# Optimization experiments

Hardware: AMD Instinct MI355X
Metric: run time of the kernel (lower is better)

Reference implementation:

```python
import jax, jax.numpy as jnp
import numpy as np
from jax import lax

T, C_IN, H, W = 15, 6, 160, 160
F1, K1, THR1 = 30, 5, 15.0
F2, K2, THR2 = 250, 3, 10.0
KWTA2, RADIUS2 = 8, 1


def conv2d(x, w):
    # x: [T, Cin, H, W] (time occupies the batch slot, SpykeTorch style); w: [Cout, Cin, k, k]
    return lax.conv_general_dilated(x, w, (1, 1), 'VALID',
                                    dimension_numbers=('NCHW', 'OIHW', 'NCHW'))


def fire(pot, thr):
    # torch.nn.functional.threshold_(pot, thr, 0): keep strictly-greater values
    p = jnp.where(pot > thr, pot, 0.0)
    return jnp.sign(p), p


def max_pool(x, k, s):
    return lax.reduce_window(x, -jnp.inf, lax.max, (1, 1, k, k), (1, 1, s, s), 'VALID')


def pad_hw(x, p):
    return jnp.pad(x, ((0, 0), (0, 0), (p, p), (p, p)))


def pointwise_inhibition(pot):
    # pot: [T, F, H, W] thresholded potentials (cumulative spike encoding over T).
    # At each spatial position keep only the feature that spiked earliest (via the
    # per-timestep max feature at the first spiking timestep); zero all others.
    t = pot.shape[0]
    max_val = pot.max(axis=1, keepdims=True)      # [T,1,H,W]
    max_idx = pot.argmax(axis=1, keepdims=True)   # [T,1,H,W]
    clamp = jnp.sign(max_val)                     # spike indicator of per-position max
    first_t = jnp.clip((t - clamp.sum(axis=0, keepdims=True)).astype(jnp.int32), 0, t - 1)
    last = clamp[-1:]                             # [1,1,H,W]: 1 if position ever spiked
    winner_f = jnp.take_along_axis(max_idx, first_t, axis=0)  # [1,1,H,W]
    f_range = jnp.arange(pot.shape[1]).reshape(1, -1, 1, 1)
    coef = jnp.where(f_range == winner_f, last, 0.0)          # scatter_(1, winners, last)
    return pot * coef


def get_k_winners(pot, spikes, kwta, radius):
    # Faithful jit-friendly version of sf.get_k_winners: rank by (spiked-early, potential),
    # iteratively pick the max, suppress its whole feature map and a (2r+1)^2 spatial
    # window across all features (NMS-like).
    t, f, h, w = pot.shape
    first_t = jnp.clip((t - spikes.sum(axis=0)).astype(jnp.int32), 0, t - 1)  # [F,H,W]
    values = jnp.take_along_axis(pot, first_t[None], axis=0)[0]  # earliest potential per neuron
    truncated = spikes * values[None]
    v = truncated.max() * t
    total = (truncated + spikes * v).sum(axis=0)  # [F,H,W]
    hs, ws = jnp.arange(h), jnp.arange(w)

    def step(tot, _):
        idx = jnp.argmax(tot)
        val = tot.reshape(-1)[idx]
        valid = val != 0.0
        fi = idx // (h * w)
        hi = (idx % (h * w)) // w
        wi = idx % w
        tot = jnp.where(valid, tot.at[fi].set(0.0), tot)  # block the winning feature
        sp = (jnp.abs(hs - hi)[:, None] <= radius) & (jnp.abs(ws - wi)[None, :] <= radius)
        tot = jnp.where(valid & sp[None], 0.0, tot)       # columnar spatial inhibition
        win = jnp.where(valid, jnp.stack([fi, hi, wi]), -1)
        return tot, win

    _, winners = lax.scan(step, total, None, length=kwta)
    return winners  # [kwta, 3] (feature, row, col), -1 rows = no winner


def setup_inputs():
    key = jax.random.key(0)
    k1, k2, k3 = jax.random.split(key, 3)
    # Cumulative spike-wave input: each (c,h,w) neuron fires at most once; spikes accumulate over T.
    u = jax.random.uniform(k1, (T, C_IN, H, W), dtype=jnp.float32)
    data = jnp.clip(jnp.cumsum((u < 0.05).astype(jnp.float32), axis=0), 0.0, 1.0)
    W1 = 0.8 + 0.05 * jax.random.normal(k2, (F1, C_IN, K1, K1), dtype=jnp.float32)
    W2 = 0.8 + 0.05 * jax.random.normal(k3, (F2, F1, K2, K2), dtype=jnp.float32)
    return {"data": data, "W1": W1, "W2": W2}


def reference(data, W1, W2):
    x = pad_hw(data, 2)                                  # sf.pad(data, (2,2,2,2))
    spike1, _ = fire(conv2d(x, W1), THR1)                # conv1 + fire(thr=15)
    inp2 = pad_hw(max_pool(spike1, 2, 2), 1)             # pool(2,2) + pad(1,1,1,1)
    _, pot2 = fire(conv2d(inp2, W2), THR2)               # conv2 + fire(thr=10)
    pot2 = pointwise_inhibition(pot2)                    # lateral inhibition
    spike2 = jnp.sign(pot2)
    winners = get_k_winners(pot2, spike2, KWTA2, RADIUS2)  # k=8, r=1 spatial k-WTA
    return spike2, pot2, winners
```

## Files before the change

kernel.cpp:

```cpp
#include <hip/hip_runtime.h>
#include <cstdint>

#define T_    15
#define C1    6
#define F1    30
#define THR1  15.0f
#define F2    250
#define THR2  10.0f
#define WP    80
#define NLOC  6400
#define KWTA  8
#define P1R   164
#define P1S   (164*164)
#define P2R   84
#define P2S   (84*84)
#define POT_OFF 24000000
#define WIN_OFF 48000000

typedef unsigned long long u64;
typedef unsigned short u16;
typedef short s16x8 __attribute__((ext_vector_type(8)));
typedef float f32x4 __attribute__((ext_vector_type(4)));

static __device__ __forceinline__ u16 f2bf(float x) {
    unsigned u = __float_as_uint(x);
    return (u16)((u + 0x7FFF + ((u >> 16) & 1)) >> 16);
}
static __device__ __forceinline__ float bf2f(u16 h) {
    return __uint_as_float(((unsigned)h) << 16);
}

__global__ void k_pad(const float* __restrict__ data, float* __restrict__ P1) {
    int idx = blockIdx.x * 256 + threadIdx.x;
    int x = idx % 160;
    int y = (idx / 160) % 160;
    int tc = idx / 25600;
    P1[(size_t)tc * P1S + (size_t)(y + 2) * P1R + (x + 2)] = data[idx];
}

__global__ __launch_bounds__(256) void k_conv1(const float* __restrict__ P1,
                                               const float* __restrict__ W1,
                                               float* __restrict__ P2) {
    int lane = threadIdx.x & 63;
    int wv   = __builtin_amdgcn_readfirstlane(threadIdx.x >> 6);
    int f    = blockIdx.y * 4 + wv;
    int fw   = f < F1 ? f : F1 - 1;
    int ty   = blockIdx.x / 5, tx = blockIdx.x % 5;
    int t    = blockIdx.z;
    int py   = lane >> 2, pxg = lane & 3;
    int rowb = 32 * ty + 2 * py;
    int cb   = 32 * tx + 8 * pxg;
    const float* p1 = P1 + (size_t)(t * C1) * P1S;

    float a0[8], a1[8];
    #pragma unroll
    for (int i = 0; i < 8; i++) { a0[i] = 0.f; a1[i] = 0.f; }

    for (int c = 0; c < C1; c++) {
        const float* pc = p1 + (size_t)c * P1S;
        const float* wc = W1 + (fw * C1 + c) * 25;
        #pragma unroll
        for (int r = 0; r < 6; r++) {
            const float4* rp = (const float4*)(pc + (size_t)(rowb + r) * P1R + cb);
            float4 u0 = rp[0], u1 = rp[1], u2 = rp[2];
            float d[12] = {u0.x,u0.y,u0.z,u0.w, u1.x,u1.y,u1.z,u1.w, u2.x,u2.y,u2.z,u2.w};
            if (r <= 4) {
                #pragma unroll
                for (int kx = 0; kx < 5; kx++) {
                    float w = wc[r * 5 + kx];
                    #pragma unroll
                    for (int cc = 0; cc < 8; cc++) a0[cc] += w * d[cc + kx];
                }
            }
            if (r >= 1) {
                #pragma unroll
                for (int kx = 0; kx < 5; kx++) {
                    float w = wc[(r - 1) * 5 + kx];
                    #pragma unroll
                    for (int cc = 0; cc < 8; cc++) a1[cc] += w * d[cc + kx];
                }
            }
        }
    }
    if (f < F1) {
        float* p2 = P2 + (size_t)(t * F1 + f) * P2S;
        int prow = 1 + 16 * ty + py;
        int pcol = 1 + 16 * tx + 4 * pxg;
        #pragma unroll
        for (int q = 0; q < 4; q++) {
            bool s = (a0[2*q] > THR1) || (a0[2*q+1] > THR1) ||
                     (a1[2*q] > THR1) || (a1[2*q+1] > THR1);
            p2[(size_t)prow * P2R + pcol + q] = s ? 1.0f : 0.0f;
        }
    }
}

__global__ void k_wprep(const float* __restrict__ W2, u16* __restrict__ Wf) {
    int E = blockIdx.x * 256 + threadIdx.x;
    int j    = E & 7;
    int lane = (E >> 3) & 63;
    int ft   = (E >> 9) & 15;
    int rest = E >> 13;
    int s = rest / 9, g = rest % 9;
    int c = (lane >> 4) * 8 + j;
    int f = ft * 16 + (lane & 15);
    float w = (c < F1 && f < F2) ? W2[f * 270 + c * 9 + g] : 0.f;
    u16 h = f2bf(w);          float fh = bf2f(h);
    u16 m = f2bf(w - fh);     float fm = bf2f(m);
    u16 l = f2bf(w - fh - fm);
    Wf[E] = (s == 0) ? h : (s == 1) ? m : l;
}

__global__ __launch_bounds__(256) void k_conv2m(const float* __restrict__ P2,
                                                const u16* __restrict__ Wf,
                                                u64* __restrict__ gkey) {
    __shared__ u16 rawT[6 * 18 * 32];
    __shared__ u64 skey[4 * 4 * 16];
    int tid  = threadIdx.x;
    int lane = tid & 63;
    int wv   = __builtin_amdgcn_readfirstlane(tid >> 6);
    int bx   = blockIdx.x;
    int t    = blockIdx.y;
    int xt = bx % 5, yt = bx / 5;
    int y0 = yt * 4, x0 = xt * 16;

    for (int e = tid; e < 3456; e += 256) {
        int c = e / 108, rem = e % 108, r = rem / 18, col = rem % 18;
        float v = (c < F1)
            ? P2[(size_t)(t * F1 + c) * P2S + (size_t)(y0 + r) * P2R + (x0 + col)] : 0.f;
        rawT[(r * 18 + col) * 32 + c] = f2bf(v);
    }
    __syncthreads();

    int q = lane >> 4, n = lane & 15;
    f32x4 accA[4][4], accB[4][4];
    #pragma unroll
    for (int j = 0; j < 4; j++)
        #pragma unroll
        for (int nt = 0; nt < 4; nt++) { accA[j][nt] = (f32x4)0.f; accB[j][nt] = (f32x4)0.f; }

    #pragma unroll
    for (int ky = 0; ky < 3; ky++) {
        #pragma unroll
        for (int kx = 0; kx < 3; kx++) {
            int g = ky * 3 + kx;
            s16x8 bf[4];
            #pragma unroll
            for (int nt = 0; nt < 4; nt++)
                bf[nt] = *(const s16x8*)&rawT[((nt + ky) * 18 + (n + kx)) * 32 + q * 8];
            #pragma unroll
            for (int s = 0; s < 3; s++) {
                #pragma unroll
                for (int j = 0; j < 4; j++) {
                    s16x8 af = *(const s16x8*)&Wf[(size_t)((((s * 9 + g) * 16) + (wv * 4 + j)) * 64 + lane) * 8];
                    f32x4* accp = (s == 0) ? accA[j] : accB[j];
                    #pragma unroll
                    for (int nt = 0; nt < 4; nt++)
                        accp[nt] = __builtin_amdgcn_mfma_f32_16x16x32_bf16(af, bf[nt], accp[nt], 0, 0, 0);
                }
            }
        }
    }

    #pragma unroll
    for (int nt = 0; nt < 4; nt++) {
        u64 best = 0;
        #pragma unroll
        for (int j = 0; j < 4; j++) {
            #pragma unroll
            for (int r = 0; r < 4; r++) {
                float pot = accA[j][nt][r] + accB[j][nt][r];
                float rr  = pot > THR2 ? pot : 0.f;
                int f = (wv * 4 + j) * 16 + q * 4 + r;
                u64 key = ((u64)__float_as_uint(rr) << 32) | (u64)(unsigned)(255 - f);
                best = best > key ? best : key;
            }
        }
        u64 o = __shfl_xor(best, 16, 64); best = best > o ? best : o;
        o     = __shfl_xor(best, 32, 64); best = best > o ? best : o;
        if (q == 0) skey[(wv * 4 + nt) * 16 + n] = best;
    }
    __syncthreads();
    if (tid < 64) {
        int nt2 = tid >> 4, n2 = tid & 15;
        u64 b = skey[nt2 * 16 + n2];
        #pragma unroll
        for (int w = 1; w < 4; w++) {
            u64 k = skey[(w * 4 + nt2) * 16 + n2];
            b = b > k ? b : k;
        }
        gkey[(size_t)t * NLOC + (size_t)(y0 + nt2) * WP + (x0 + n2)] = b;
    }
}

__global__ void k_col(const u64* __restrict__ gkey, const float* __restrict__ P2,
                      const float* __restrict__ W2, int* __restrict__ winf,
                      float* __restrict__ colv) {
    int idx = blockIdx.x * 256 + threadIdx.x;
    int t   = idx / NLOC;
    int loc = idx % NLOC;
    float mv[T_]; int mi[T_];
    #pragma unroll
    for (int t2 = 0; t2 < T_; t2++) {
        u64 k = gkey[(size_t)t2 * NLOC + loc];
        mv[t2] = __uint_as_float((unsigned)(k >> 32));
        mi[t2] = 255 - (int)(k & 0xFFFFFFFFu);
    }
    int nclamp = 0;
    #pragma unroll
    for (int t2 = 0; t2 < T_; t2++) nclamp += (mv[t2] > 0.f);
    int ft = T_ - nclamp; if (ft > T_ - 1) ft = T_ - 1;
    int wf = -1;
    #pragma unroll
    for (int t2 = 0; t2 < T_; t2++) if (t2 == ft) wf = mi[t2];
    if (!(mv[T_ - 1] > 0.f)) wf = -1;
    if (t == 0) winf[loc] = wf;

    float acc = 0.f;
    if (wf >= 0) {
        int y = loc / WP, x = loc % WP;
        const float* pb = P2 + (size_t)(t * F1) * P2S + (size_t)y * P2R + x;
        const float* wb = W2 + wf * 270;
        for (int c = 0; c < F1; c++) {
            #pragma unroll
            for (int ky = 0; ky < 3; ky++)
                #pragma unroll
                for (int kx = 0; kx < 3; kx++)
                    acc += wb[c * 9 + ky * 3 + kx] * pb[(size_t)c * P2S + ky * P2R + kx];
    }
    }
    acc = acc > THR2 ? acc : 0.f;
    colv[t * NLOC + loc] = acc;
}

__global__ void k_stat(const float* __restrict__ colv, int* __restrict__ nsA,
                       float* __restrict__ vfA, unsigned* __restrict__ vmax) {
    int loc = blockIdx.x * 256 + threadIdx.x;
    float col[T_];
    #pragma unroll
    for (int t = 0; t < T_; t++) col[t] = colv[t * NLOC + loc];
    int ns = 0;
    #pragma unroll
    for (int t = 0; t < T_; t++) ns += (col[t] > 0.f);
    int f2 = T_ - ns; if (f2 > T_ - 1) f2 = T_ - 1;
    float vf = 0.f;
    #pragma unroll
    for (int t = 0; t < T_; t++) if (t == f2) vf = col[t];
    nsA[loc] = ns; vfA[loc] = vf;
    atomicMax(vmax, __float_as_uint(vf));
}

__global__ void k_zero(float* __restrict__ outbuf, const int* __restrict__ winf,
                       const float* __restrict__ colv) {
    int idx = blockIdx.x * 256 + threadIdx.x;
    if (idx >= T_ * F2 * (NLOC / 4)) return;
    int l4 = idx % (NLOC / 4);
    int f  = (idx / (NLOC / 4)) % F2;
    int t  = idx / ((NLOC / 4) * F2);
    int loc = l4 * 4;
    int4   wf = *(const int4*)(winf + loc);
    float4 cv = *(const float4*)(colv + t * NLOC + loc);
    float4 po, sp;
    po.x = (wf.x == f) ? cv.x : 0.f;  sp.x = po.x > 0.f ? 1.f : 0.f;
    po.y = (wf.y == f) ? cv.y : 0.f;  sp.y = po.y > 0.f ? 1.f : 0.f;
    po.z = (wf.z == f) ? cv.z : 0.f;  sp.z = po.z > 0.f ? 1.f : 0.f;
    po.w = (wf.w == f) ? cv.w : 0.f;  sp.w = po.w > 0.f ? 1.f : 0.f;
    size_t off = ((size_t)t * F2 + f) * NLOC + loc;
    *(float4*)(outbuf + POT_OFF + off) = po;
    *(float4*)(outbuf + off) = sp;
}

__global__ __launch_bounds__(256) void k_winners(const int* __restrict__ winf,
                                                 const int* __restrict__ nsA,
                                                 const float* __restrict__ vfA,
                                                 const unsigned* __restrict__ vmax,
                                                 float* __restrict__ wout) {
    __shared__ float tot[NLOC];
    __shared__ int   wfl[NLOC];
    __shared__ float rv[256];
    __shared__ int   rk[256];
    __shared__ float bvS; __shared__ int fiS, hiS, wiS;
    int tid = threadIdx.x;
    float v = __uint_as_float(vmax[0]) * (float)T_;
    for (int l = tid; l < NLOC; l += 256) {
        tot[l] = (float)nsA[l] * (vfA[l] + v);
        wfl[l] = winf[l];
    }
    __syncthreads();
    for (int it = 0; it < KWTA; it++) {
        float bv = 0.f; int bk = 0x7fffffff;
        #pragma unroll
        for (int i = 0; i < 25; i++) {
            int l = tid * 25 + i;
            float vv = tot[l];
            int k = wfl[l] * NLOC + l;
            if (vv > bv || (vv == bv && k < bk)) { bv = vv; bk = k; }
        }
        rv[tid] = bv; rk[tid] = bk;
        __syncthreads();
        for (int s = 128; s > 0; s >>= 1) {
            if (tid < s) {
                float v2 = rv[tid + s]; int k2 = rk[tid + s];
                if (v2 > rv[tid] || (v2 == rv[tid] && k2 < rk[tid])) { rv[tid] = v2; rk[tid] = k2; }
            }
            __syncthreads();
        }
        if (tid == 0) {
            float bvv = rv[0]; int bkk = rk[0];
            bool valid = bvv > 0.f;
            int fi = valid ? bkk / NLOC : -1;
            int lc = bkk % NLOC;
            int hi = valid ? lc / WP : -1;
            int wi = valid ? lc % WP : -1;
            wout[it * 3 + 0] = (float)fi;
            wout[it * 3 + 1] = (float)hi;
            wout[it * 3 + 2] = (float)wi;
            bvS = bvv; fiS = fi; hiS = hi; wiS = wi;
        }
        __syncthreads();
        if (bvS > 0.f) {
            #pragma unroll
            for (int i = 0; i < 25; i++) {
                int l = tid * 25 + i;
                int h = l / WP, w = l % WP;
                bool kill = (wfl[l] == fiS) ||
                            (h >= hiS - 1 && h <= hiS + 1 && w >= wiS - 1 && w <= wiS + 1);
                if (kill) tot[l] = 0.f;
            }
        }
        __syncthreads();
    }
}

extern "C" void kernel_launch(void* const* d_in, const int* in_sizes, int n_in,
                              void* d_out, int out_size, void* d_ws, size_t ws_size,
                              hipStream_t stream) {
    const float* data = (const float*)d_in[0];
    const float* W1   = (const float*)d_in[1];
    const float* W2   = (const float*)d_in[2];
    float* out = (float*)d_out;
    float* ws  = (float*)d_ws;

    float*    P1   = ws;
    float*    P2   = ws + 2420640;
    u16*      Wf   = (u16*)(ws + 5595840);
    int*      winf = (int*)(ws + 5706432);
    int*      nsA  = (int*)(ws + 5712832);
    float*    vfA  = ws + 5719232;
    float*    colv = ws + 5725632;
    unsigned* vmax = (unsigned*)(ws + 5821632);

    u64* gkey = (u64*)d_out;

    hipMemsetAsync(P1, 0, 2420640 * sizeof(float), stream);
    hipMemsetAsync(P2, 0, 3175200 * sizeof(float), stream);
    hipMemsetAsync(vmax, 0, sizeof(unsigned), stream);

    k_pad    <<<9000, 256, 0, stream>>>(data, P1);
    k_conv1  <<<dim3(25, 8, T_), 256, 0, stream>>>(P1, W1, P2);
    k_wprep  <<<864, 256, 0, stream>>>(W2, Wf);
    k_conv2m <<<dim3(100, T_), 256, 0, stream>>>(P2, Wf, gkey);
    k_col    <<<375, 256, 0, stream>>>(gkey, P2, W2, winf, colv);
    k_stat   <<<25, 256, 0, stream>>>(colv, nsA, vfA, vmax);
    k_zero   <<<(T_ * F2 * (NLOC / 4) + 255) / 256, 256, 0, stream>>>(out, winf, colv);
    k_winners<<<1, 256, 0, stream>>>(winf, nsA, vfA, vmax, out + WIN_OFF);
}
```

Measured before the change: 410.1 us.

## Move conv1 to split-bf16 MFMA with fused padding, pooling, and near-threshold fixup

The separate pad kernel and the FP32 scalar conv1 are replaced by one MFMA-based conv1 that reads the raw input into shared memory with implicit zero padding, stores bf16 copies, and writes 2x2-pooled spikes directly. Weights are split into three bf16 terms for accuracy. Pooled cells whose potentials fall near the threshold are queued via an atomic counter and recomputed in FP32 by a new fixup kernel. conv2's shared-memory layout is also reorganised into channel groups of eight, which likely reduces LDS bank conflicts. The P1 buffer and its memset go away, at the cost of an extra launch and a bounded fixup list that could overflow.

```diff
diff --git a/kernel.cpp b/kernel.cpp
--- a/kernel.cpp
+++ b/kernel.cpp
@@ -10,12 +10,12 @@
 #define WP    80
 #define NLOC  6400
 #define KWTA  8
-#define P1R   164
-#define P1S   (164*164)
 #define P2R   84
 #define P2S   (84*84)
 #define POT_OFF 24000000
 #define WIN_OFF 48000000
+#define EPS1  1e-2f
+#define FIXCAP 65536
 
 typedef unsigned long long u64;
 typedef unsigned short u16;
@@ -30,105 +30,193 @@
     return __uint_as_float(((unsigned)h) << 16);
 }
 
-__global__ void k_pad(const float* __restrict__ data, float* __restrict__ P1) {
-    int idx = blockIdx.x * 256 + threadIdx.x;
-    int x = idx % 160;
-    int y = (idx / 160) % 160;
-    int tc = idx / 25600;
-    P1[(size_t)tc * P1S + (size_t)(y + 2) * P1R + (x + 2)] = data[idx];
-}
-
-__global__ __launch_bounds__(256) void k_conv1(const float* __restrict__ P1,
-                                               const float* __restrict__ W1,
-                                               float* __restrict__ P2) {
-    int lane = threadIdx.x & 63;
-    int wv   = __builtin_amdgcn_readfirstlane(threadIdx.x >> 6);
-    int f    = blockIdx.y * 4 + wv;
-    int fw   = f < F1 ? f : F1 - 1;
-    int ty   = blockIdx.x / 5, tx = blockIdx.x % 5;
-    int t    = blockIdx.z;
-    int py   = lane >> 2, pxg = lane & 3;
-    int rowb = 32 * ty + 2 * py;
-    int cb   = 32 * tx + 8 * pxg;
-    const float* p1 = P1 + (size_t)(t * C1) * P1S;
-
-    float a0[8], a1[8];
-    #pragma unroll
-    for (int i = 0; i < 8; i++) { a0[i] = 0.f; a1[i] = 0.f; }
-
-    for (int c = 0; c < C1; c++) {
-        const float* pc = p1 + (size_t)c * P1S;
-        const float* wc = W1 + (fw * C1 + c) * 25;
-        #pragma unroll
-        for (int r = 0; r < 6; r++) {
-            const float4* rp = (const float4*)(pc + (size_t)(rowb + r) * P1R + cb);
-            float4 u0 = rp[0], u1 = rp[1], u2 = rp[2];
-            float d[12] = {u0.x,u0.y,u0.z,u0.w, u1.x,u1.y,u1.z,u1.w, u2.x,u2.y,u2.z,u2.w};
-            if (r <= 4) {
+__global__ void k_wprep(const float* __restrict__ W2, const float* __restrict__ W1,
+                        u16* __restrict__ Wf2, u16* __restrict__ Wf1) {
+    int b = blockIdx.x;
+    if (b < 864) {
+        int E = b * 256 + threadIdx.x;
+        int j    = E & 7;
+        int lane = (E >> 3) & 63;
+        int ft   = (E >> 9) & 15;
+        int rest = E >> 13;
+        int s = rest / 9, g = rest % 9;
+        int c = (lane >> 4) * 8 + j;
+        int f = ft * 16 + (lane & 15);
+        float w = (c < F1 && f < F2) ? W2[f * 270 + c * 9 + g] : 0.f;
+        u16 h = f2bf(w);          float fh = bf2f(h);
+        u16 m = f2bf(w - fh);     float fm = bf2f(m);
+        u16 l = f2bf(w - fh - fm);
+        Wf2[E] = (s == 0) ? h : (s == 1) ? m : l;
+    } else {
+        int E = (b - 864) * 256 + threadIdx.x;
+        int j    = E & 7;
+        int lane = (E >> 3) & 63;
+        int ft   = (E >> 9) & 1;
+        int sf   = E >> 10;
+        int s = sf % 7, sp = sf / 7;
+        int q = lane >> 4, m15 = lane & 15;
+        int f  = ft * 16 + m15;
+        int kp = s * 4 + q;
+        int c  = j;
+        float w = 0.f;
+        if (f < F1 && kp < 25 && c < C1) {
+            int ky = kp / 5, kx = kp % 5;
+            w = W1[((f * C1 + c) * 5 + ky) * 5 + kx];
+        }
+        u16 h = f2bf(w);          float fh = bf2f(h);
+        u16 m = f2bf(w - fh);     float fm = bf2f(m);
+        u16 l = f2bf(w - fh - fm);
+        Wf1[E] = (sp == 0) ? h : (sp == 1) ? m : l;
+    }
+}
+
+__global__ __launch_bounds__(256) void k_conv1m(const float* __restrict__ data,
+                                                const u16* __restrict__ Wf1,
+                                                float* __restrict__ P2,
+                                                int* __restrict__ cnt,
+                                                int* __restrict__ list) {
+    __shared__ u16 strip[3200];
+    __shared__ unsigned char pooled[2048];
+    int tid  = threadIdx.x;
+    int lane = tid & 63;
+    int wv   = __builtin_amdgcn_readfirstlane(tid >> 6);
+    int t    = blockIdx.y;
+    int xt = blockIdx.x % 10, yt = blockIdx.x / 10;
+    int x0 = xt * 16, y0 = yt * 16;
+
+    for (int e = tid; e < 3200; e += 256) {
+        int c = e / 400, r = (e / 20) % 20, cl = e % 20;
+        int yy = y0 + r - 2, xx = x0 + cl - 2;
+        float v = 0.f;
+        if (c < C1 && yy >= 0 && yy < 160 && xx >= 0 && xx < 160)
+            v = data[(size_t)(t * C1 + c) * 25600 + yy * 160 + xx];
+        strip[(r * 20 + cl) * 8 + c] = f2bf(v);
+    }
+    __syncthreads();
+
+    int q = lane >> 4, n = lane & 15;
+    f32x4 acc[2][4];
+    #pragma unroll
+    for (int j = 0; j < 2; j++)
+        #pragma unroll
+        for (int nt = 0; nt < 4; nt++) acc[j][nt] = (f32x4)0.f;
+
+    #pragma unroll
+    for (int s = 0; s < 7; s++) {
+        int kp = s * 4 + q;
+        int ky = 0, kx = 0;
+        if (kp < 25) { ky = kp / 5; kx = kp - ky * 5; }
+        s16x8 bf[4];
+        #pragma unroll
+        for (int nt = 0; nt < 4; nt++)
+            bf[nt] = *(const s16x8*)&strip[((wv * 4 + nt + ky) * 20 + (n + kx)) * 8];
+        #pragma unroll
+        for (int sp = 0; sp < 3; sp++) {
+            #pragma unroll
+            for (int j = 0; j < 2; j++) {
+                s16x8 af = *(const s16x8*)&Wf1[(size_t)(((sp * 7 + s) * 2 + j) * 64 + lane) * 8];
                 #pragma unroll
-                for (int kx = 0; kx < 5; kx++) {
-                    float w = wc[r * 5 + kx];
+                for (int nt = 0; nt < 4; nt++)
+                    acc[j][nt] = __builtin_amdgcn_mfma_f32_16x16x32_bf16(af, bf[nt], acc[j][nt], 0, 0, 0);
+            }
+        }
+    }
+
+    unsigned sb[4], nf[4];
+    #pragma unroll
+    for (int nt = 0; nt < 4; nt++) {
+        unsigned s8 = 0, fl = 0;
+        #pragma unroll
+        for (int j = 0; j < 2; j++)
+            #pragma unroll
+            for (int r = 0; r < 4; r++) {
+                float p = acc[j][nt][r];
+                s8 |= (p > THR1 ? 1u : 0u) << (j * 4 + r);
+                fl |= (fabsf(p - THR1) < EPS1 ? 1u : 0u);
+            }
+        sb[nt] = s8; nf[nt] = fl;
+    }
+    #pragma unroll
+    for (int nt = 0; nt < 4; nt++) {
+        sb[nt] |= (unsigned)__shfl_xor((int)sb[nt], 1, 64);
+        nf[nt] |= (unsigned)__shfl_xor((int)nf[nt], 1, 64);
+    }
+    unsigned p0 = sb[0] | sb[1], p1 = sb[2] | sb[3];
+    unsigned fw = (nf[0] | nf[1]) | ((nf[2] | nf[3]) << 1);
+    fw |= (unsigned)__shfl_xor((int)fw, 16, 64);
+    fw |= (unsigned)__shfl_xor((int)fw, 32, 64);
+    if (!(n & 1)) {
+        int px = n >> 1;
+        #pragma unroll
+        for (int j = 0; j < 2; j++)
+            #pragma unroll
+            for (int r = 0; r < 4; r++) {
+                int f = j * 16 + q * 4 + r;
+                pooled[((wv * 2 + 0) * 8 + px) * 32 + f] = (p0 >> (j * 4 + r)) & 1;
+                pooled[((wv * 2 + 1) * 8 + px) * 32 + f] = (p1 >> (j * 4 + r)) & 1;
+            }
+        if (q == 0 && fw) {
+            int cb = t * NLOC + (yt * 8) * WP + (xt * 8 + px);
+            if (fw & 1) { int id = atomicAdd(cnt, 1); if (id < FIXCAP) list[id] = cb + (wv * 2 + 0) * WP; }
+            if (fw & 2) { int id = atomicAdd(cnt, 1); if (id < FIXCAP) list[id] = cb + (wv * 2 + 1) * WP; }
+        }
+    }
+    __syncthreads();
+    for (int i = tid; i < 1920; i += 256) {
+        int f = i >> 6, pos = i & 63, py = pos >> 3, px = pos & 7;
+        P2[(size_t)(t * F1 + f) * P2S + (size_t)(1 + yt * 8 + py) * P2R + (1 + xt * 8 + px)]
+            = pooled[pos * 32 + f] ? 1.f : 0.f;
+    }
+}
+
+__global__ void k_fix(const float* __restrict__ data, const float* __restrict__ W1,
+                      float* __restrict__ P2, const int* __restrict__ list,
+                      const int* __restrict__ cnt) {
+    int m = *cnt; if (m > FIXCAP) m = FIXCAP;
+    int nitems = m * F1;
+    for (int i = blockIdx.x * 256 + threadIdx.x; i < nitems; i += gridDim.x * 256) {
+        int cell = list[i / F1], f = i % F1;
+        int t = cell / NLOC, rem = cell % NLOC, py = rem / WP, px = rem % WP;
+        bool s = false;
+        #pragma unroll
+        for (int dy = 0; dy < 2; dy++)
+            #pragma unroll
+            for (int dx = 0; dx < 2; dx++) {
+                int y = 2 * py + dy, x = 2 * px + dx;
+                float acc = 0.f;
+                for (int c = 0; c < C1; c++)
                     #pragma unroll
-                    for (int cc = 0; cc < 8; cc++) a0[cc] += w * d[cc + kx];
-                }
-            }
-            if (r >= 1) {
-                #pragma unroll
-                for (int kx = 0; kx < 5; kx++) {
-                    float w = wc[(r - 1) * 5 + kx];
-                    #pragma unroll
-                    for (int cc = 0; cc < 8; cc++) a1[cc] += w * d[cc + kx];
-                }
-            }
-        }
-    }
-    if (f < F1) {
-        float* p2 = P2 + (size_t)(t * F1 + f) * P2S;
-        int prow = 1 + 16 * ty + py;
-        int pcol = 1 + 16 * tx + 4 * pxg;
-        #pragma unroll
-        for (int q = 0; q < 4; q++) {
-            bool s = (a0[2*q] > THR1) || (a0[2*q+1] > THR1) ||
-                     (a1[2*q] > THR1) || (a1[2*q+1] > THR1);
-            p2[(size_t)prow * P2R + pcol + q] = s ? 1.0f : 0.0f;
-        }
-    }
-}
-
-__global__ void k_wprep(const float* __restrict__ W2, u16* __restrict__ Wf) {
-    int E = blockIdx.x * 256 + threadIdx.x;
-    int j    = E & 7;
-    int lane = (E >> 3) & 63;
-    int ft   = (E >> 9) & 15;
-    int rest = E >> 13;
-    int s = rest / 9, g = rest % 9;
-    int c = (lane >> 4) * 8 + j;
-    int f = ft * 16 + (lane & 15);
-    float w = (c < F1 && f < F2) ? W2[f * 270 + c * 9 + g] : 0.f;
-    u16 h = f2bf(w);          float fh = bf2f(h);
-    u16 m = f2bf(w - fh);     float fm = bf2f(m);
-    u16 l = f2bf(w - fh - fm);
-    Wf[E] = (s == 0) ? h : (s == 1) ? m : l;
+                    for (int ky = 0; ky < 5; ky++)
+                        #pragma unroll
+                        for (int kx = 0; kx < 5; kx++) {
+                            int yy = y + ky - 2, xx = x + kx - 2;
+                            float v = (yy >= 0 && yy < 160 && xx >= 0 && xx < 160)
+                                ? data[(size_t)(t * C1 + c) * 25600 + yy * 160 + xx] : 0.f;
+                            acc += W1[((f * C1 + c) * 5 + ky) * 5 + kx] * v;
+                        }
+                s |= acc > THR1;
+            }
+        P2[(size_t)(t * F1 + f) * P2S + (size_t)(1 + py) * P2R + (1 + px)] = s ? 1.f : 0.f;
+    }
 }
 
 __global__ __launch_bounds__(256) void k_conv2m(const float* __restrict__ P2,
                                                 const u16* __restrict__ Wf,
                                                 u64* __restrict__ gkey) {
-    __shared__ u16 rawT[6 * 18 * 32];
-    __shared__ u64 skey[4 * 4 * 16];
+    __shared__ u16 rawT[3456];
+    __shared__ u64 skey[256];
     int tid  = threadIdx.x;
     int lane = tid & 63;
     int wv   = __builtin_amdgcn_readfirstlane(tid >> 6);
-    int bx   = blockIdx.x;
     int t    = blockIdx.y;
-    int xt = bx % 5, yt = bx / 5;
+    int xt = blockIdx.x % 5, yt = blockIdx.x / 5;
     int y0 = yt * 4, x0 = xt * 16;
 
     for (int e = tid; e < 3456; e += 256) {
-        int c = e / 108, rem = e % 108, r = rem / 18, col = rem % 18;
+        int c = e / 108, r = (e / 18) % 6, col = e % 18;
         float v = (c < F1)
             ? P2[(size_t)(t * F1 + c) * P2S + (size_t)(y0 + r) * P2R + (x0 + col)] : 0.f;
-        rawT[(r * 18 + col) * 32 + c] = f2bf(v);
+        rawT[((r * 4 + (c >> 3)) * 18 + col) * 8 + (c & 7)] = f2bf(v);
     }
     __syncthreads();
 
@@ -147,16 +235,21 @@
             s16x8 bf[4];
             #pragma unroll
             for (int nt = 0; nt < 4; nt++)
-                bf[nt] = *(const s16x8*)&rawT[((nt + ky) * 18 + (n + kx)) * 32 + q * 8];
+                bf[nt] = *(const s16x8*)&rawT[(((nt + ky) * 4 + q) * 18 + (n + kx)) * 8];
             #pragma unroll
             for (int s = 0; s < 3; s++) {
                 #pragma unroll
                 for (int j = 0; j < 4; j++) {
                     s16x8 af = *(const s16x8*)&Wf[(size_t)((((s * 9 + g) * 16) + (wv * 4 + j)) * 64 + lane) * 8];
-                    f32x4* accp = (s == 0) ? accA[j] : accB[j];
-                    #pragma unroll
-                    for (int nt = 0; nt < 4; nt++)
-                        accp[nt] = __builtin_amdgcn_mfma_f32_16x16x32_bf16(af, bf[nt], accp[nt], 0, 0, 0);
+                    if (s == 0) {
+                        #pragma unroll
+                        for (int nt = 0; nt < 4; nt++)
+                            accA[j][nt] = __builtin_amdgcn_mfma_f32_16x16x32_bf16(af, bf[nt], accA[j][nt], 0, 0, 0);
+                    } else {
+                        #pragma unroll
+                        for (int nt = 0; nt < 4; nt++)
+                            accB[j][nt] = __builtin_amdgcn_mfma_f32_16x16x32_bf16(af, bf[nt], accB[j][nt], 0, 0, 0);
+                    }
                 }
             }
         }
@@ -183,13 +276,13 @@
     __syncthreads();
     if (tid < 64) {
         int nt2 = tid >> 4, n2 = tid & 15;
-        u64 b = skey[nt2 * 16 + n2];
+        u64 bk = skey[nt2 * 16 + n2];
         #pragma unroll
         for (int w = 1; w < 4; w++) {
             u64 k = skey[(w * 4 + nt2) * 16 + n2];
-            b = b > k ? b : k;
-        }
-        gkey[(size_t)t * NLOC + (size_t)(y0 + nt2) * WP + (x0 + n2)] = b;
+            bk = bk > k ? bk : k;
+        }
+        gkey[(size_t)t * NLOC + (size_t)(y0 + nt2) * WP + (x0 + n2)] = bk;
     }
 }
 
@@ -227,7 +320,7 @@
                 #pragma unroll
                 for (int kx = 0; kx < 3; kx++)
                     acc += wb[c * 9 + ky * 3 + kx] * pb[(size_t)c * P2S + ky * P2R + kx];
-    }
+        }
     }
     acc = acc > THR2 ? acc : 0.f;
     colv[t * NLOC + loc] = acc;
@@ -341,25 +434,26 @@
     float* out = (float*)d_out;
     float* ws  = (float*)d_ws;
 
-    float*    P1   = ws;
-    float*    P2   = ws + 2420640;
-    u16*      Wf   = (u16*)(ws + 5595840);
-    int*      winf = (int*)(ws + 5706432);
-    int*      nsA  = (int*)(ws + 5712832);
-    float*    vfA  = ws + 5719232;
-    float*    colv = ws + 5725632;
-    unsigned* vmax = (unsigned*)(ws + 5821632);
+    float*    P2   = ws;
+    u16*      Wf2  = (u16*)(ws + 3175200);
+    u16*      Wf1  = (u16*)(ws + 3285792);
+    int*      winf = (int*)(ws + 3296544);
+    int*      nsA  = (int*)(ws + 3302944);
+    float*    vfA  = ws + 3309344;
+    float*    colv = ws + 3315744;
+    unsigned* vmax = (unsigned*)(ws + 3411744);
+    int*      cnt  = (int*)(ws + 3411745);
+    int*      list = (int*)(ws + 3411746);
 
     u64* gkey = (u64*)d_out;
 
-    hipMemsetAsync(P1, 0, 2420640 * sizeof(float), stream);
     hipMemsetAsync(P2, 0, 3175200 * sizeof(float), stream);
-    hipMemsetAsync(vmax, 0, sizeof(unsigned), stream);
-
-    k_pad    <<<9000, 256, 0, stream>>>(data, P1);
-    k_conv1  <<<dim3(25, 8, T_), 256, 0, stream>>>(P1, W1, P2);
-    k_wprep  <<<864, 256, 0, stream>>>(W2, Wf);
-    k_conv2m <<<dim3(100, T_), 256, 0, stream>>>(P2, Wf, gkey);
+    hipMemsetAsync(vmax, 0, 2 * sizeof(unsigned), stream);
+
+    k_wprep  <<<948, 256, 0, stream>>>(W2, W1, Wf2, Wf1);
+    k_conv1m <<<dim3(100, T_), 256, 0, stream>>>(data, Wf1, P2, cnt, list);
+    k_fix    <<<120, 256, 0, stream>>>(data, W1, P2, list, cnt);
+    k_conv2m <<<dim3(100, T_), 256, 0, stream>>>(P2, Wf2, gkey);
     k_col    <<<375, 256, 0, stream>>>(gkey, P2, W2, winf, colv);
     k_stat   <<<25, 256, 0, stream>>>(colv, nsA, vfA, vmax);
     k_zero   <<<(T_ * F2 * (NLOC / 4) + 255) / 256, 256, 0, stream>>>(out, winf, colv);
```

New measurement: 468.1 us. +14.1%, slower.
